# Kernel optimization log

Measured on AMD Instinct MI355X. Metric: run time of the kernel, lower is better.

## Reference

```python
import jax, jax.numpy as jnp
import numpy as np

B, IN, C, H, E = 8192, 768, 64, 64, 16  # batch, input_dim, n_concepts, hidden_dim, embedding_dim


def setup_inputs() -> dict:
    key = jax.random.key(0)
    ks = jax.random.split(key, 10)

    def w(k, shape, fan_in):
        return jax.random.normal(k, shape, jnp.float32) / np.float32(np.sqrt(fan_in))

    inp = {"x": jax.random.normal(ks[0], (B, IN), jnp.float32)}
    i = 1
    for pre, din, dout in (("pos", IN, E), ("neg", IN, E), ("cp", 2 * E, 1)):
        inp[pre + "_W1"] = w(ks[i], (C, din, H), din)
        inp[pre + "_b1"] = jnp.zeros((C, H), jnp.float32)
        inp[pre + "_W2"] = w(ks[i + 1], (C, H, H), H)
        inp[pre + "_b2"] = jnp.zeros((C, H), jnp.float32)
        inp[pre + "_W3"] = w(ks[i + 2], (C, H, dout), H)
        inp[pre + "_b3"] = jnp.zeros((C, dout), jnp.float32)
        i += 3
    return inp


def _bank(x, W1, b1, W2, b2, W3, b3):
    # x: [B, IN]; per-concept MLP batched over C via einsum -> [B, C, E]
    h = jax.nn.relu(jnp.einsum('bi,cih->bch', x, W1) + b1)
    h = jax.nn.relu(jnp.einsum('bch,cho->bco', h, W2) + b2)
    return jnp.einsum('bch,che->bce', h, W3) + b3


def reference(x, pos_W1, pos_b1, pos_W2, pos_b2, pos_W3, pos_b3,
              neg_W1, neg_b1, neg_W2, neg_b2, neg_W3, neg_b3,
              cp_W1, cp_b1, cp_W2, cp_b2, cp_W3, cp_b3):
    pos = _bank(x, pos_W1, pos_b1, pos_W2, pos_b2, pos_W3, pos_b3)  # [B,C,E]
    neg = _bank(x, neg_W1, neg_b1, neg_W2, neg_b2, neg_W3, neg_b3)  # [B,C,E]
    # torch cat([pos, neg], dim=1) on [B,E,C], then x[:,:,i] -> per-concept [B, 2E]
    xc = jnp.concatenate([pos, neg], axis=-1)  # [B,C,2E]
    h = jax.nn.relu(jnp.einsum('bci,cih->bch', xc, cp_W1) + cp_b1)
    h = jax.nn.relu(jnp.einsum('bch,cho->bco', h, cp_W2) + cp_b2)
    concepts = (jnp.einsum('bch,cho->bco', h, cp_W3) + cp_b3)[..., 0]  # [B,C]
    w = jnp.clip(concepts * 0.5 + 0.5, 0.0, 1.0)[:, :, None]  # gate in [0,1]
    emb = pos * w + neg * (1.0 - w)  # [B,C,E]
    # torch layout is [B,E,C] then .view(B,-1): transpose before flattening
    emb_flat = jnp.transpose(emb, (0, 2, 1)).reshape(x.shape[0], E * C)
    return emb_flat, concepts
```

## Files before the change

### kernel.cpp

```cpp
#include <hip/hip_runtime.h>
#include <hip/hip_bf16.h>


#define B_   8192
#define IN_  768
#define C_   64
#define H_   64
#define E_   16
#define BM_  128

typedef __bf16 bf16x8 __attribute__((ext_vector_type(8)));
typedef float  f32x4  __attribute__((ext_vector_type(4)));

__device__ __forceinline__ f32x4 mfma16(bf16x8 a, bf16x8 b, f32x4 c) {
  return __builtin_amdgcn_mfma_f32_16x16x32_bf16(a, b, c, 0, 0, 0);
}

__device__ __forceinline__ bf16x8 cvt8(float4 a, float4 b) {
  bf16x8 r;
  r[0] = (__bf16)a.x; r[1] = (__bf16)a.y; r[2] = (__bf16)a.z; r[3] = (__bf16)a.w;
  r[4] = (__bf16)b.x; r[5] = (__bf16)b.y; r[6] = (__bf16)b.z; r[7] = (__bf16)b.w;
  return r;
}

__device__ __forceinline__ void zero_acc(f32x4 (&acc)[2][4]) {
  const f32x4 z = {0.f, 0.f, 0.f, 0.f};
#pragma unroll
  for (int mt = 0; mt < 2; ++mt)
#pragma unroll
    for (int nt = 0; nt < 4; ++nt) acc[mt][nt] = z;
}

struct __align__(16) SmemT {
  __bf16 hb[BM_ * 72];
  __bf16 wt[64 * 72];
  __bf16 xcb[BM_ * 40];
  float  conc[BM_];
};
static_assert(sizeof(SmemT) <= 40960, "LDS overflow");

__device__ __forceinline__ void epi72(__bf16* __restrict__ hb, f32x4 (&acc)[2][4],
                                      const float* __restrict__ bias,
                                      int wave, int quad, int l16) {
#pragma unroll
  for (int nt = 0; nt < 4; ++nt) {
    const int col = nt * 16 + l16;
    const float bv = bias[col];
#pragma unroll
    for (int mt = 0; mt < 2; ++mt)
#pragma unroll
      for (int r = 0; r < 4; ++r) {
        int row = wave * 32 + mt * 16 + quad * 4 + r;
        hb[row * 72 + col] = (__bf16)fmaxf(acc[mt][nt][r] + bv, 0.f);
      }
  }
}

__device__ __forceinline__ void gemm64(const __bf16* __restrict__ hb,
                                       const __bf16* __restrict__ wt,
                                       f32x4 (&acc)[2][4], int wave, int quad, int l16) {
#pragma unroll
  for (int ks = 0; ks < 2; ++ks) {
    bf16x8 a[2], bb[4];
#pragma unroll
    for (int mt = 0; mt < 2; ++mt)
      a[mt] = *(const bf16x8*)(hb + (wave * 32 + mt * 16 + l16) * 72 + ks * 32 + quad * 8);
#pragma unroll
    for (int nt = 0; nt < 4; ++nt)
      bb[nt] = *(const bf16x8*)(wt + (nt * 16 + l16) * 72 + ks * 32 + quad * 8);
#pragma unroll
    for (int mt = 0; mt < 2; ++mt)
#pragma unroll
      for (int nt = 0; nt < 4; ++nt)
        acc[mt][nt] = mfma16(a[mt], bb[nt], acc[mt][nt]);
  }
}

__device__ __forceinline__ void stage_w64(const __bf16* __restrict__ Wt,
                                          __bf16* __restrict__ wt, int tid) {
#pragma unroll
  for (int it = 0; it < 2; ++it) {
    int q = tid + it * 256;
    int n = q >> 3, i = q & 7;
    *(uint4*)&wt[n * 72 + i * 8] = *(const uint4*)(Wt + n * 64 + i * 8);
  }
}

__device__ __forceinline__ void run_bank_t(SmemT& sm, const __bf16* __restrict__ af,
    const __bf16* __restrict__ W1k, const float* __restrict__ b1,
    const __bf16* __restrict__ W2t, const float* __restrict__ b2,
    const __bf16* __restrict__ W3t, const float* __restrict__ b3,
    int xc_off, int tid, int wave, int quad, int l16)
{
  __bf16* wt = sm.wt;
  __bf16* hb = sm.hb;

  f32x4 acc1[2][4]; zero_acc(acc1);
  for (int kt = 0; kt < IN_ / 64; ++kt) {
    stage_w64(W1k + kt * 4096, wt, tid);
    __syncthreads();
#pragma unroll
    for (int ks = 0; ks < 2; ++ks) {
      bf16x8 a[2], bb[4];
#pragma unroll
      for (int mt = 0; mt < 2; ++mt)
        a[mt] = *(const bf16x8*)(af + ((kt * 2 + ks) * 2 + mt) * 512);
#pragma unroll
      for (int nt = 0; nt < 4; ++nt)
        bb[nt] = *(const bf16x8*)&wt[(nt * 16 + l16) * 72 + ks * 32 + quad * 8];
#pragma unroll
      for (int mt = 0; mt < 2; ++mt)
#pragma unroll
        for (int nt = 0; nt < 4; ++nt)
          acc1[mt][nt] = mfma16(a[mt], bb[nt], acc1[mt][nt]);
    }
    __syncthreads();
  }
  epi72(hb, acc1, b1, wave, quad, l16);
  stage_w64(W2t, wt, tid);
  __syncthreads();

  f32x4 acc2[2][4]; zero_acc(acc2);
  gemm64(hb, wt, acc2, wave, quad, l16);
  __syncthreads();
  epi72(hb, acc2, b2, wave, quad, l16);
  if (tid < 128)
    *(uint4*)&wt[(tid >> 3) * 72 + (tid & 7) * 8] =
        *(const uint4*)(W3t + (tid >> 3) * 64 + (tid & 7) * 8);
  __syncthreads();

  f32x4 acc3[2];
  { const f32x4 z = {0.f, 0.f, 0.f, 0.f}; acc3[0] = z; acc3[1] = z; }
#pragma unroll
  for (int ks = 0; ks < 2; ++ks) {
    bf16x8 bb = *(const bf16x8*)&wt[l16 * 72 + ks * 32 + quad * 8];
#pragma unroll
    for (int mt = 0; mt < 2; ++mt) {
      bf16x8 a = *(const bf16x8*)&hb[(wave * 32 + mt * 16 + l16) * 72 + ks * 32 + quad * 8];
      acc3[mt] = mfma16(a, bb, acc3[mt]);
    }
  }
  {
    float bv = b3[l16];
#pragma unroll
    for (int mt = 0; mt < 2; ++mt)
#pragma unroll
      for (int r = 0; r < 4; ++r) {
        int row = wave * 32 + mt * 16 + quad * 4 + r;
        sm.xcb[row * 40 + xc_off + l16] = (__bf16)(acc3[mt][r] + bv);
      }
  }
  __syncthreads();
}

__global__ __launch_bounds__(256, 4) void cb_fused_t(
    const __bf16* __restrict__ xfrag,
    const __bf16* __restrict__ pW1t, const float* __restrict__ pb1,
    const __bf16* __restrict__ pW2t, const float* __restrict__ pb2,
    const __bf16* __restrict__ pW3t, const float* __restrict__ pb3,
    const __bf16* __restrict__ nW1t, const float* __restrict__ nb1,
    const __bf16* __restrict__ nW2t, const float* __restrict__ nb2,
    const __bf16* __restrict__ nW3t, const float* __restrict__ nb3,
    const __bf16* __restrict__ cW1t, const float* __restrict__ cb1,
    const __bf16* __restrict__ cW2t, const float* __restrict__ cb2,
    const __bf16* __restrict__ cw3,  const float* __restrict__ cb3,
    float* __restrict__ out_emb, float* __restrict__ out_con)
{
  __shared__ SmemT sm;
  const int tid  = threadIdx.x;
  const int wave = tid >> 6, lane = tid & 63;
  const int quad = lane >> 4, l16 = lane & 15;
  const int row0 = blockIdx.x * BM_;
  const int c    = blockIdx.y;
  __bf16* hb = sm.hb;
  __bf16* wt = sm.wt;

  const __bf16* af = xfrag + ((size_t)(blockIdx.x * 4 + wave)) * 24576 + (size_t)lane * 8;

  run_bank_t(sm, af, pW1t + (size_t)c * 49152, pb1 + c * 64,
             pW2t + (size_t)c * 4096, pb2 + c * 64,
             pW3t + (size_t)c * 1024, pb3 + c * 16,
             0, tid, wave, quad, l16);
  run_bank_t(sm, af, nW1t + (size_t)c * 49152, nb1 + c * 64,
             nW2t + (size_t)c * 4096, nb2 + c * 64,
             nW3t + (size_t)c * 1024, nb3 + c * 16,
             16, tid, wave, quad, l16);

  {
    int n = tid >> 2, i = tid & 3;
    *(uint4*)&wt[n * 72 + i * 8] = *(const uint4*)(cW1t + ((size_t)c * 64 + n) * 32 + i * 8);
  }
  __syncthreads();
  f32x4 acc1[2][4]; zero_acc(acc1);
  {
    bf16x8 a[2], bb[4];
#pragma unroll
    for (int mt = 0; mt < 2; ++mt)
      a[mt] = *(const bf16x8*)&sm.xcb[(wave * 32 + mt * 16 + l16) * 40 + quad * 8];
#pragma unroll
    for (int nt = 0; nt < 4; ++nt)
      bb[nt] = *(const bf16x8*)&wt[(nt * 16 + l16) * 72 + quad * 8];
#pragma unroll
    for (int mt = 0; mt < 2; ++mt)
#pragma unroll
      for (int nt = 0; nt < 4; ++nt)
        acc1[mt][nt] = mfma16(a[mt], bb[nt], acc1[mt][nt]);
  }
  __syncthreads();
  epi72(hb, acc1, cb1 + c * 64, wave, quad, l16);
  stage_w64(cW2t + (size_t)c * 4096, wt, tid);
  __syncthreads();

  f32x4 acc2[2][4]; zero_acc(acc2);
  gemm64(hb, wt, acc2, wave, quad, l16);
  __syncthreads();
  epi72(hb, acc2, cb2 + c * 64, wave, quad, l16);
  if (tid < 8) *(uint4*)&wt[tid * 8] = *(const uint4*)(cw3 + (size_t)c * 64 + tid * 8);
  __syncthreads();

  f32x4 acc3[2];
  { const f32x4 z = {0.f, 0.f, 0.f, 0.f}; acc3[0] = z; acc3[1] = z; }
#pragma unroll
  for (int ks = 0; ks < 2; ++ks) {
    bf16x8 bb = {};
    if (l16 == 0) bb = *(const bf16x8*)&wt[ks * 32 + quad * 8];
#pragma unroll
    for (int mt = 0; mt < 2; ++mt) {
      bf16x8 a = *(const bf16x8*)&hb[(wave * 32 + mt * 16 + l16) * 72 + ks * 32 + quad * 8];
      acc3[mt] = mfma16(a, bb, acc3[mt]);
    }
  }
  if (l16 == 0) {
    float bv = cb3[c];
#pragma unroll
    for (int mt = 0; mt < 2; ++mt)
#pragma unroll
      for (int r = 0; r < 4; ++r)
        sm.conc[wave * 32 + mt * 16 + quad * 4 + r] = acc3[mt][r] + bv;
  }
  __syncthreads();

  for (int ii = tid; ii < BM_ * E_; ii += 256) {
    int row = ii >> 4, e = ii & 15;
    float cv = sm.conc[row];
    float w  = fminf(fmaxf(cv * 0.5f + 0.5f, 0.f), 1.f);
    float pv2 = (float)sm.xcb[row * 40 + e];
    float nv2 = (float)sm.xcb[row * 40 + 16 + e];
    out_emb[(size_t)(row0 + row) * (E_ * C_) + e * C_ + c] = pv2 * w + nv2 * (1.f - w);
  }
  if (tid < 128) out_con[(size_t)(row0 + tid) * C_ + c] = sm.conc[tid];
}

#define TSEG 5
#define PSEG 4
struct PrepArgs {
  const float* tsrc[TSEG];
  __bf16*      tdst[TSEG];
  int tstart[TSEG + 1];
  int ktiles[TSEG];
  const float* xsrc;
  __bf16*      xdst;
  const float* psrc[PSEG];
  __bf16*      pdst[PSEG];
  int pstart[PSEG + 1];
  int pchunks[PSEG];
  int kdiv8[PSEG];
  int N[PSEG];
  int tblocks;
};

__global__ __launch_bounds__(256) void prep_all(PrepArgs a) {
  const int tid = threadIdx.x;
  const int b = blockIdx.x;
  __shared__ __bf16 lt[64 * 72];
  if (b < a.tblocks) {
    int s = 0;
    while (s < TSEG - 1 && b >= a.tstart[s + 1]) ++s;
    const int idx = b - a.tstart[s];
    const int kt = idx % a.ktiles[s];
    const int c  = idx / a.ktiles[s];
    const int K  = a.ktiles[s] * 64;
    const float* src = a.tsrc[s] + (size_t)c * K * 64 + (size_t)kt * 64 * 64;
    __bf16*      dst = a.tdst[s] + ((size_t)c * a.ktiles[s] + kt) * 4096;
    const int r = tid >> 4, c4 = (tid & 15) * 4;
#pragma unroll
    for (int it = 0; it < 4; ++it) {
      int k = r + it * 16;
      float4 v = *(const float4*)(src + (size_t)k * 64 + c4);
      lt[(c4 + 0) * 72 + k] = (__bf16)v.x;
      lt[(c4 + 1) * 72 + k] = (__bf16)v.y;
      lt[(c4 + 2) * 72 + k] = (__bf16)v.z;
      lt[(c4 + 3) * 72 + k] = (__bf16)v.w;
    }
    __syncthreads();
    const int n = tid >> 3, i = tid & 7;
#pragma unroll
    for (int it = 0; it < 2; ++it) {
      int nn = n + it * 32;
      *(uint4*)(dst + nn * 64 + i * 8) = *(const uint4*)&lt[nn * 72 + i * 8];
    }
  } else if (b < a.tblocks + 256) {
    const int rt  = b - a.tblocks;
    const int l16 = tid & 15, quad = (tid >> 4) & 3, mt = (tid >> 6) & 1, ks = tid >> 7;
    const float* srow = a.xsrc + ((size_t)rt * 32 + mt * 16 + l16) * IN_ + ks * 32 + quad * 8;
    __bf16* drow = a.xdst + (size_t)rt * 24576 + ((size_t)ks * 2 + mt) * 512
                 + (size_t)(quad * 16 + l16) * 8;
#pragma unroll
    for (int kt = 0; kt < 12; ++kt) {
      const float* s = srow + kt * 64;
      float4 v0 = *(const float4*)s, v1 = *(const float4*)(s + 4);
      *(uint4*)(drow + (size_t)kt * 2048) = __builtin_bit_cast(uint4, cvt8(v0, v1));
    }
  } else {
    const int bb = b - a.tblocks - 256;
    int s = 0;
    while (s < PSEG - 1 && bb >= a.pstart[s + 1]) ++s;
    const int lb  = bb - a.pstart[s];
    const int nch = a.pchunks[s];
    const int kc  = a.kdiv8[s];
    const int N   = a.N[s];
#pragma unroll
    for (int j = 0; j < 4; ++j) {
      const int li = (lb * 4 + j) * 256 + tid;
      if (li >= nch) break;
      if (N == 1) {
        const float4* src = (const float4*)a.psrc[s] + (size_t)li * 2;
        float4 v0 = src[0], v1 = src[1];
        *(uint4*)(a.pdst[s] + (size_t)li * 8) = __builtin_bit_cast(uint4, cvt8(v0, v1));
      } else {
        int rn = li / kc;
        int k0 = (li - rn * kc) * 8;
        int cc = rn / N;
        int n  = rn - cc * N;
        const float* src = a.psrc[s] + ((size_t)cc * kc * 8 + k0) * N + n;
        bf16x8 r;
#pragma unroll
        for (int jj = 0; jj < 8; ++jj) r[jj] = (__bf16)src[(size_t)jj * N];
        *(uint4*)(a.pdst[s] + (size_t)rn * kc * 8 + k0) = __builtin_bit_cast(uint4, r);
      }
    }
  }
}

extern "C" void kernel_launch(void* const* d_in, const int* in_sizes, int n_in,
                              void* d_out, int out_size, void* d_ws, size_t ws_size,
                              hipStream_t stream) {
  const float* xf   = (const float*)d_in[0];
  const float* pW1f = (const float*)d_in[1];
  const float* pb1f = (const float*)d_in[2];
  const float* pW2f = (const float*)d_in[3];
  const float* pb2f = (const float*)d_in[4];
  const float* pW3f = (const float*)d_in[5];
  const float* pb3f = (const float*)d_in[6];
  const float* nW1f = (const float*)d_in[7];
  const float* nb1f = (const float*)d_in[8];
  const float* nW2f = (const float*)d_in[9];
  const float* nb2f = (const float*)d_in[10];
  const float* nW3f = (const float*)d_in[11];
  const float* nb3f = (const float*)d_in[12];
  const float* cW1f = (const float*)d_in[13];
  const float* cb1f = (const float*)d_in[14];
  const float* cW2f = (const float*)d_in[15];
  const float* cb2f = (const float*)d_in[16];
  const float* cW3f = (const float*)d_in[17];
  const float* cb3f = (const float*)d_in[18];

  float* out_emb = (float*)d_out;
  float* out_con = out_emb + (size_t)B_ * E_ * C_;

  const int cx   = B_ * IN_;
  const int cW1c = C_ * IN_ * H_;
  const int cW2c = C_ * H_ * H_;
  const int cW3c = C_ * H_ * E_;
  const int ccW1 = C_ * 2 * E_ * H_;
  const int ccW3 = C_ * H_;

  __bf16* w = (__bf16*)d_ws;
  size_t o = 0;
  __bf16* xfr  = w + o; o += cx;
  __bf16* pw1t = w + o; o += cW1c;
  __bf16* nw1t = w + o; o += cW1c;
  __bf16* pw2t = w + o; o += cW2c;
  __bf16* nw2t = w + o; o += cW2c;
  __bf16* cw2t = w + o; o += cW2c;
  __bf16* pw3t = w + o; o += cW3c;
  __bf16* nw3t = w + o; o += cW3c;
  __bf16* cw1t = w + o; o += ccW1;
  __bf16* cw3w = w + o; o += ccW3;

  PrepArgs a;
  int tb = 0, pb = 0;
  {
    const float* tsrc[TSEG] = {pW1f, nW1f, pW2f, nW2f, cW2f};
    __bf16*      tdst[TSEG] = {pw1t, nw1t, pw2t, nw2t, cw2t};
    const int    tk[TSEG]   = {12,   12,   1,    1,    1};
    for (int i = 0; i < TSEG; ++i) {
      a.tsrc[i] = tsrc[i]; a.tdst[i] = tdst[i]; a.ktiles[i] = tk[i];
      a.tstart[i] = tb;
      tb += tk[i] * C_;
    }
    a.tstart[TSEG] = tb;
    a.tblocks = tb;

    a.xsrc = xf;
    a.xdst = xfr;

    const float* psrc[PSEG] = {cW3f, pW3f, nW3f, cW1f};
    __bf16*      pdst[PSEG] = {cw3w, pw3t, nw3t, cw1t};
    const int    pKs[PSEG]  = {0,    64,   64,   32};
    const int    pNs[PSEG]  = {1,    16,   16,   64};
    const int    pels[PSEG] = {ccW3, cW3c, cW3c, ccW1};
    for (int i = 0; i < PSEG; ++i) {
      a.psrc[i] = psrc[i]; a.pdst[i] = pdst[i];
      a.pchunks[i] = pels[i] / 8;
      a.kdiv8[i] = (pNs[i] == 1) ? (pels[i] / 8) : (pKs[i] / 8);
      a.N[i] = pNs[i];
      a.pstart[i] = pb;
      pb += (pels[i] / 8 + 1023) / 1024;
    }
    a.pstart[PSEG] = pb;
  }
  prep_all<<<tb + 256 + pb, 256, 0, stream>>>(a);

  dim3 grid(B_ / BM_, C_);
  cb_fused_t<<<grid, 256, 0, stream>>>(xfr,
      pw1t, pb1f, pw2t, pb2f, pw3t, pb3f,
      nw1t, nb1f, nw2t, nb2f, nw3t, nb3f,
      cw1t, cb1f, cw2t, cb2f, cw3w, cb3f,
      out_emb, out_con);
}
```

Before: 367.2 us.

## Stage x and W1 tiles into LDS via async global_load_lds with XOR swizzle

The layer-1 GEMM previously read x fragments straight from global memory into registers and staged W1 through registers into padded LDS. Now both the x tile and the W1 tile are copied into LDS with global_load_lds direct-to-LDS loads, using an XOR-swizzled unpadded layout to avoid bank conflicts. The prep kernel is changed to write x and W1 in that pre-swizzled layout, and the LDS is reorganised into a union buffer. The copies are still synchronous per k-tile with no double buffering, so load latency is not hidden, and every block now reloads x into LDS instead of reading it from cache into registers.

```diff
diff --git a/kernel.cpp b/kernel.cpp
--- a/kernel.cpp
+++ b/kernel.cpp
@@ -23,6 +23,12 @@
   return r;
 }
 
+__device__ __forceinline__ void async16(const __bf16* g, __bf16* l) {
+  __builtin_amdgcn_global_load_lds(
+      (const __attribute__((address_space(1))) unsigned int*)(const void*)g,
+      (__attribute__((address_space(3))) unsigned int*)(void*)l, 16, 0, 0);
+}
+
 __device__ __forceinline__ void zero_acc(f32x4 (&acc)[2][4]) {
   const f32x4 z = {0.f, 0.f, 0.f, 0.f};
 #pragma unroll
@@ -32,12 +38,11 @@
 }
 
 struct __align__(16) SmemT {
-  __bf16 hb[BM_ * 72];
-  __bf16 wt[64 * 72];
+  __bf16 u[13824];
   __bf16 xcb[BM_ * 40];
   float  conc[BM_];
 };
-static_assert(sizeof(SmemT) <= 40960, "LDS overflow");
+static_assert(sizeof(SmemT) == 38400 - 0 * 512 + 512 * 0 + 0 ? true : sizeof(SmemT) <= 40960, "LDS overflow");
 
 __device__ __forceinline__ void epi72(__bf16* __restrict__ hb, f32x4 (&acc)[2][4],
                                       const float* __restrict__ bias,
@@ -86,28 +91,40 @@
   }
 }
 
-__device__ __forceinline__ void run_bank_t(SmemT& sm, const __bf16* __restrict__ af,
+__device__ __forceinline__ void run_bank_t(SmemT& sm, const __bf16* __restrict__ gx,
     const __bf16* __restrict__ W1k, const float* __restrict__ b1,
     const __bf16* __restrict__ W2t, const float* __restrict__ b2,
     const __bf16* __restrict__ W3t, const float* __restrict__ b3,
-    int xc_off, int tid, int wave, int quad, int l16)
+    int xc_off, int tid, int wave, int lane, int quad, int l16)
 {
-  __bf16* wt = sm.wt;
-  __bf16* hb = sm.hb;
+  __bf16* xs  = sm.u;
+  __bf16* wt1 = sm.u + 8192;
+  __bf16* hb  = sm.u;
+  __bf16* wtt = sm.u + 9216;
+  const int x7 = l16 & 7;
 
   f32x4 acc1[2][4]; zero_acc(acc1);
   for (int kt = 0; kt < IN_ / 64; ++kt) {
-    stage_w64(W1k + kt * 4096, wt, tid);
+    const __bf16* gxt = gx + (size_t)kt * 8192;
+    const __bf16* gwt = W1k + (size_t)kt * 4096;
+#pragma unroll
+    for (int i = 0; i < 4; ++i)
+      async16(gxt + (((wave * 4 + i) * 64 + lane) * 8), xs + (wave * 4 + i) * 512);
+#pragma unroll
+    for (int i = 0; i < 2; ++i)
+      async16(gwt + (((wave * 2 + i) * 64 + lane) * 8), wt1 + (wave * 2 + i) * 512);
     __syncthreads();
 #pragma unroll
     for (int ks = 0; ks < 2; ++ks) {
       bf16x8 a[2], bb[4];
 #pragma unroll
       for (int mt = 0; mt < 2; ++mt)
-        a[mt] = *(const bf16x8*)(af + ((kt * 2 + ks) * 2 + mt) * 512);
+        a[mt] = *(const bf16x8*)&xs[(wave * 32 + mt * 16 + l16) * 64
+                                    + (((ks * 4 + quad) ^ x7) * 8)];
 #pragma unroll
       for (int nt = 0; nt < 4; ++nt)
-        bb[nt] = *(const bf16x8*)&wt[(nt * 16 + l16) * 72 + ks * 32 + quad * 8];
+        bb[nt] = *(const bf16x8*)&wt1[(nt * 16 + l16) * 64
+                                      + (((ks * 4 + quad) ^ x7) * 8)];
 #pragma unroll
       for (int mt = 0; mt < 2; ++mt)
 #pragma unroll
@@ -117,15 +134,15 @@
     __syncthreads();
   }
   epi72(hb, acc1, b1, wave, quad, l16);
-  stage_w64(W2t, wt, tid);
+  stage_w64(W2t, wtt, tid);
   __syncthreads();
 
   f32x4 acc2[2][4]; zero_acc(acc2);
-  gemm64(hb, wt, acc2, wave, quad, l16);
+  gemm64(hb, wtt, acc2, wave, quad, l16);
   __syncthreads();
   epi72(hb, acc2, b2, wave, quad, l16);
   if (tid < 128)
-    *(uint4*)&wt[(tid >> 3) * 72 + (tid & 7) * 8] =
+    *(uint4*)&wtt[(tid >> 3) * 72 + (tid & 7) * 8] =
         *(const uint4*)(W3t + (tid >> 3) * 64 + (tid & 7) * 8);
   __syncthreads();
 
@@ -133,7 +150,7 @@
   { const f32x4 z = {0.f, 0.f, 0.f, 0.f}; acc3[0] = z; acc3[1] = z; }
 #pragma unroll
   for (int ks = 0; ks < 2; ++ks) {
-    bf16x8 bb = *(const bf16x8*)&wt[l16 * 72 + ks * 32 + quad * 8];
+    bf16x8 bb = *(const bf16x8*)&wtt[l16 * 72 + ks * 32 + quad * 8];
 #pragma unroll
     for (int mt = 0; mt < 2; ++mt) {
       bf16x8 a = *(const bf16x8*)&hb[(wave * 32 + mt * 16 + l16) * 72 + ks * 32 + quad * 8];
@@ -172,23 +189,23 @@
   const int quad = lane >> 4, l16 = lane & 15;
   const int row0 = blockIdx.x * BM_;
   const int c    = blockIdx.y;
-  __bf16* hb = sm.hb;
-  __bf16* wt = sm.wt;
-
-  const __bf16* af = xfrag + ((size_t)(blockIdx.x * 4 + wave)) * 24576 + (size_t)lane * 8;
-
-  run_bank_t(sm, af, pW1t + (size_t)c * 49152, pb1 + c * 64,
+  __bf16* hb  = sm.u;
+  __bf16* wtt = sm.u + 9216;
+
+  const __bf16* gx = xfrag + (size_t)blockIdx.x * (12 * 8192);
+
+  run_bank_t(sm, gx, pW1t + (size_t)c * 49152, pb1 + c * 64,
              pW2t + (size_t)c * 4096, pb2 + c * 64,
              pW3t + (size_t)c * 1024, pb3 + c * 16,
-             0, tid, wave, quad, l16);
-  run_bank_t(sm, af, nW1t + (size_t)c * 49152, nb1 + c * 64,
+             0, tid, wave, lane, quad, l16);
+  run_bank_t(sm, gx, nW1t + (size_t)c * 49152, nb1 + c * 64,
              nW2t + (size_t)c * 4096, nb2 + c * 64,
              nW3t + (size_t)c * 1024, nb3 + c * 16,
-             16, tid, wave, quad, l16);
+             16, tid, wave, lane, quad, l16);
 
   {
     int n = tid >> 2, i = tid & 3;
-    *(uint4*)&wt[n * 72 + i * 8] = *(const uint4*)(cW1t + ((size_t)c * 64 + n) * 32 + i * 8);
+    *(uint4*)&wtt[n * 72 + i * 8] = *(const uint4*)(cW1t + ((size_t)c * 64 + n) * 32 + i * 8);
   }
   __syncthreads();
   f32x4 acc1[2][4]; zero_acc(acc1);
@@ -199,7 +216,7 @@
       a[mt] = *(const bf16x8*)&sm.xcb[(wave * 32 + mt * 16 + l16) * 40 + quad * 8];
 #pragma unroll
     for (int nt = 0; nt < 4; ++nt)
-      bb[nt] = *(const bf16x8*)&wt[(nt * 16 + l16) * 72 + quad * 8];
+      bb[nt] = *(const bf16x8*)&wtt[(nt * 16 + l16) * 72 + quad * 8];
 #pragma unroll
     for (int mt = 0; mt < 2; ++mt)
 #pragma unroll
@@ -208,14 +225,14 @@
   }
   __syncthreads();
   epi72(hb, acc1, cb1 + c * 64, wave, quad, l16);
-  stage_w64(cW2t + (size_t)c * 4096, wt, tid);
+  stage_w64(cW2t + (size_t)c * 4096, wtt, tid);
   __syncthreads();
 
   f32x4 acc2[2][4]; zero_acc(acc2);
-  gemm64(hb, wt, acc2, wave, quad, l16);
+  gemm64(hb, wtt, acc2, wave, quad, l16);
   __syncthreads();
   epi72(hb, acc2, cb2 + c * 64, wave, quad, l16);
-  if (tid < 8) *(uint4*)&wt[tid * 8] = *(const uint4*)(cw3 + (size_t)c * 64 + tid * 8);
+  if (tid < 8) *(uint4*)&wtt[tid * 8] = *(const uint4*)(cw3 + (size_t)c * 64 + tid * 8);
   __syncthreads();
 
   f32x4 acc3[2];
@@ -223,7 +240,7 @@
 #pragma unroll
   for (int ks = 0; ks < 2; ++ks) {
     bf16x8 bb = {};
-    if (l16 == 0) bb = *(const bf16x8*)&wt[ks * 32 + quad * 8];
+    if (l16 == 0) bb = *(const bf16x8*)&wtt[ks * 32 + quad * 8];
 #pragma unroll
     for (int mt = 0; mt < 2; ++mt) {
       bf16x8 a = *(const bf16x8*)&hb[(wave * 32 + mt * 16 + l16) * 72 + ks * 32 + quad * 8];
@@ -258,6 +275,7 @@
   __bf16*      tdst[TSEG];
   int tstart[TSEG + 1];
   int ktiles[TSEG];
+  int swz[TSEG];
   const float* xsrc;
   __bf16*      xdst;
   const float* psrc[PSEG];
@@ -294,25 +312,28 @@
     }
     __syncthreads();
     const int n = tid >> 3, i = tid & 7;
+    const int sw = a.swz[s];
 #pragma unroll
     for (int it = 0; it < 2; ++it) {
       int nn = n + it * 32;
-      *(uint4*)(dst + nn * 64 + i * 8) = *(const uint4*)&lt[nn * 72 + i * 8];
-    }
-  } else if (b < a.tblocks + 256) {
-    const int rt  = b - a.tblocks;
-    const int l16 = tid & 15, quad = (tid >> 4) & 3, mt = (tid >> 6) & 1, ks = tid >> 7;
-    const float* srow = a.xsrc + ((size_t)rt * 32 + mt * 16 + l16) * IN_ + ks * 32 + quad * 8;
-    __bf16* drow = a.xdst + (size_t)rt * 24576 + ((size_t)ks * 2 + mt) * 512
-                 + (size_t)(quad * 16 + l16) * 8;
-#pragma unroll
-    for (int kt = 0; kt < 12; ++kt) {
-      const float* s = srow + kt * 64;
+      int ii = sw ? (i ^ (nn & 7)) : i;
+      *(uint4*)(dst + nn * 64 + ii * 8) = *(const uint4*)&lt[nn * 72 + i * 8];
+    }
+  } else if (b < a.tblocks + 768) {
+    const int idx = b - a.tblocks;
+    const int kt = idx % 12, bx = idx / 12;
+    __bf16* dst = a.xdst + ((size_t)bx * 12 + kt) * 8192;
+#pragma unroll
+    for (int i = 0; i < 4; ++i) {
+      const int cidx = i * 256 + tid;
+      const int row = cidx >> 3, phys = cidx & 7;
+      const int jj = phys ^ (row & 7);
+      const float* s = a.xsrc + ((size_t)bx * 128 + row) * IN_ + kt * 64 + jj * 8;
       float4 v0 = *(const float4*)s, v1 = *(const float4*)(s + 4);
-      *(uint4*)(drow + (size_t)kt * 2048) = __builtin_bit_cast(uint4, cvt8(v0, v1));
+      *(uint4*)(dst + (size_t)cidx * 8) = __builtin_bit_cast(uint4, cvt8(v0, v1));
     }
   } else {
-    const int bb = b - a.tblocks - 256;
+    const int bb = b - a.tblocks - 768;
     int s = 0;
     while (s < PSEG - 1 && bb >= a.pstart[s + 1]) ++s;
     const int lb  = bb - a.pstart[s];
@@ -394,8 +415,9 @@
     const float* tsrc[TSEG] = {pW1f, nW1f, pW2f, nW2f, cW2f};
     __bf16*      tdst[TSEG] = {pw1t, nw1t, pw2t, nw2t, cw2t};
     const int    tk[TSEG]   = {12,   12,   1,    1,    1};
+    const int    tsw[TSEG]  = {1,    1,    0,    0,    0};
     for (int i = 0; i < TSEG; ++i) {
-      a.tsrc[i] = tsrc[i]; a.tdst[i] = tdst[i]; a.ktiles[i] = tk[i];
+      a.tsrc[i] = tsrc[i]; a.tdst[i] = tdst[i]; a.ktiles[i] = tk[i]; a.swz[i] = tsw[i];
       a.tstart[i] = tb;
       tb += tk[i] * C_;
     }
@@ -420,7 +442,7 @@
     }
     a.pstart[PSEG] = pb;
   }
-  prep_all<<<tb + 256 + pb, 256, 0, stream>>>(a);
+  prep_all<<<tb + 768 + pb, 256, 0, stream>>>(a);
 
   dim3 grid(B_ / BM_, C_);
   cb_fused_t<<<grid, 256, 0, stream>>>(xfr,
```

Result: no change. 372.3 us (+1.4%).
